# Optimization experiments

Hardware: AMD Instinct MI355X
Metric: run time of the kernel (lower is better)

Reference implementation:

```python
import jax, jax.numpy as jnp
import numpy as np

INF_MIN = -10000.0
B, S, VOCAB = 256, 1024, 126
T = VOCAB + 2           # tag_size
START, END = T - 2, T - 1


def setup_inputs() -> dict:
    key = jax.random.key(0)
    k1, k2, k3 = jax.random.split(key, 3)
    features = jax.random.normal(k1, (B, S, T), dtype=jnp.float32)
    batch_len = jax.random.randint(k2, (B,), 1, S + 1, dtype=jnp.int32)
    transitions = jax.random.normal(k3, (T, T), dtype=jnp.float32)
    # CRF structural constraints set at init: nothing transitions INTO start,
    # nothing transitions OUT of end.
    transitions = transitions.at[:, START].set(INF_MIN).at[END, :].set(INF_MIN)
    return {"features": features, "batch_len": batch_len, "transitions": transitions}


def reference(features, batch_len, transitions):
    # features: [B, S, T], batch_len: [B], transitions: [T, T]
    b, s, t = features.shape
    alpha0 = jnp.full((b, t), INF_MIN, dtype=features.dtype).at[:, START].set(0.0)
    feats_t = jnp.transpose(features, (1, 0, 2))  # [S, B, T]

    def step(carry, feats):
        alpha, rem = carry
        # score[b, i, j] = emit[b, i] + trans[i, j] + alpha[b, j]
        scores = feats[:, :, None] + transitions[None, :, :] + alpha[:, None, :]
        alpha_next = jax.nn.logsumexp(scores, axis=2)  # [B, T]
        alive = (rem > 0)[:, None]
        alpha = jnp.where(alive, alpha_next, alpha)
        return (alpha, rem - 1), None

    (alpha, _), _ = jax.lax.scan(step, (alpha0, batch_len), feats_t)
    alpha = alpha + transitions[END][None, :]
    return jax.nn.logsumexp(alpha, axis=1)  # [B]
```

## Files before the change

kernel.cpp:

```cpp
#include <hip/hip_runtime.h>

#define BB 256
#define SS 1024
#define TT 128
#define ST 126
#define EN 127
#define IMIN -10000.0f
#define L2E 1.4426950408889634f
#define LN2f 0.6931471805599453f
#define QS 40

__global__ __launch_bounds__(512, 1) void crf_fwd(const float* __restrict__ feats,
                                                  const int* __restrict__ blen,
                                                  const float* __restrict__ trans,
                                                  float* __restrict__ out)
{
    const int tid = threadIdx.x;
    const int i   = tid >> 2;
    const int q   = tid & 3;
    const int b   = blockIdx.x;

    __shared__ __align__(16) float vbuf[2][4 * QS];
    __shared__ __align__(16) float featbuf[2][8 * TT];
    __shared__ __align__(16) float wout[TT];
    __shared__ __align__(16) float red[8];

    const float* fb = feats + (size_t)b * (SS * TT);
    const int L = blen[b];

    *(float2*)(&featbuf[0][tid * 2]) = *(const float2*)(fb + tid * 2);
    float f0 = fb[i];

    float4 P[8];
    {
        const float* trow = trans + i * TT + q * 32;
        #pragma unroll
        for (int k = 0; k < 8; ++k) {
            float4 tv = *(const float4*)(trow + 4 * k);
            P[k].x = tv.x * L2E; P[k].y = tv.y * L2E;
            P[k].z = tv.z * L2E; P[k].w = tv.w * L2E;
        }
    }
    float rm = -3.4e38f;
    #pragma unroll
    for (int k = 0; k < 8; ++k)
        rm = fmaxf(rm, fmaxf(fmaxf(P[k].x, P[k].y), fmaxf(P[k].z, P[k].w)));
    rm = fmaxf(rm, __shfl_xor(rm, 1));
    rm = fmaxf(rm, __shfl_xor(rm, 2));

    float S = 0.f;
    #pragma unroll
    for (int k = 0; k < 8; ++k) {
        P[k].x = exp2f(P[k].x - rm); P[k].y = exp2f(P[k].y - rm);
        P[k].z = exp2f(P[k].z - rm); P[k].w = exp2f(P[k].w - rm);
        S += (P[k].x + P[k].y) + (P[k].z + P[k].w);
    }
    S += __shfl_xor(S, 1);
    S += __shfl_xor(S, 2);

    float rmc = fmaxf(rm, 0.f);
    float A1 = fmaf(f0, L2E, (IMIN * L2E) + rmc +
                    log2f(fmaf(S, exp2f(rm - rmc), exp2f(-rmc))));

    if (tid == 0) red[0] = A1;
    __syncthreads();
    float sh = red[0];
    if (q == 0) vbuf[0][(i >> 5) * QS + (i & 31)] = exp2f(A1 - sh);
    __syncthreads();

    int cur = 0;
    float2 fnx = *(const float2*)(fb + 8 * TT + tid * 2);

    for (int ch = 0; ; ++ch) {
        if (8 * ch + 8 < L) {
            *(float2*)(&featbuf[(ch + 1) & 1][tid * 2]) = fnx;
            int cn = min(8 * ch + 16, SS - 8);
            fnx = *(const float2*)(fb + cn * TT + tid * 2);
        }
        const int sLo = (ch == 0) ? 1 : 8 * ch;
        const int sHi = min(8 * ch + 8, L);
        for (int s = sLo; s < sHi; ++s) {
            const float* vb = &vbuf[cur][q * QS];
            float v0f = vbuf[cur][0];
            float fv  = featbuf[ch & 1][((s & 7) << 7) + i];
            float dsh = log2f(v0f);
            float cf  = exp2f(fmaf(fv, L2E, rm - dsh));

            float a0 = 0.f, a1 = 0.f, a2 = 0.f, a3 = 0.f;
            #pragma unroll
            for (int k = 0; k < 8; ++k) {
                float4 vv = *(const float4*)(vb + 4 * k);
                a0 = fmaf(P[k].x, vv.x, a0);
                a1 = fmaf(P[k].y, vv.y, a1);
                a2 = fmaf(P[k].z, vv.z, a2);
                a3 = fmaf(P[k].w, vv.w, a3);
            }
            float part = (a0 + a1) + (a2 + a3);
            part += __shfl_xor(part, 1);
            part += __shfl_xor(part, 2);

            float vn = cf * part;
            sh += dsh;
            if (q == 0) vbuf[cur ^ 1][(i >> 5) * QS + (i & 31)] = vn;
            __syncthreads();
            cur ^= 1;
        }
        if (8 * ch + 8 >= L) break;
    }

    float vL = vbuf[cur][(i >> 5) * QS + (i & 31)];
    float w  = fmaf(trans[EN * TT + i], L2E, sh + log2f(vL));
    if (q == 0) wout[i] = w;
    __syncthreads();
    if (tid < 64) {
        float w0 = wout[tid], w1 = wout[tid + 64];
        float mm = fmaxf(w0, w1);
        #pragma unroll
        for (int off = 1; off < 64; off <<= 1) mm = fmaxf(mm, __shfl_xor(mm, off));
        float ss = exp2f(w0 - mm) + exp2f(w1 - mm);
        #pragma unroll
        for (int off = 1; off < 64; off <<= 1) ss += __shfl_xor(ss, off);
        if (tid == 0) out[b] = (mm + log2f(ss)) * LN2f;
    }
}

extern "C" void kernel_launch(void* const* d_in, const int* in_sizes, int n_in,
                              void* d_out, int out_size, void* d_ws, size_t ws_size,
                              hipStream_t stream) {
    const float* feats = (const float*)d_in[0];
    const int*   blen  = (const int*)d_in[1];
    const float* trans = (const float*)d_in[2];
    float*       o     = (float*)d_out;
    crf_fwd<<<dim3(BB), dim3(512), 0, stream>>>(feats, blen, trans, o);
}
```

Measured before the change: 372.3 us.

## Rewrite CRF forward as single-wavefront kernel with fp16 dot2 and DPP reductions

Each batch item now runs on one 64-lane wavefront. Every lane owns two tag rows and keeps the exp-transition matrix packed as fp16 pairs in registers, computing the row dot products with v_dot2_f32_f16. This removes block-wide __syncthreads, shared feature staging and cross-lane partial sums from every time step. Per-step normalization uses a wave-wide max via DPP and shuffles, and the next feature is prefetched directly from global memory. The change risks fp16 precision loss in the transition and alpha values, and adds high register pressure from 128 packed registers per lane.

```diff
diff --git a/kernel.cpp b/kernel.cpp
--- a/kernel.cpp
+++ b/kernel.cpp
@@ -3,125 +3,152 @@
 #define BB 256
 #define SS 1024
 #define TT 128
-#define ST 126
 #define EN 127
 #define IMIN -10000.0f
 #define L2E 1.4426950408889634f
 #define LN2f 0.6931471805599453f
-#define QS 40
 
-__global__ __launch_bounds__(512, 1) void crf_fwd(const float* __restrict__ feats,
-                                                  const int* __restrict__ blen,
-                                                  const float* __restrict__ trans,
-                                                  float* __restrict__ out)
+typedef _Float16 half2v __attribute__((ext_vector_type(2)));
+
+__device__ __forceinline__ float fdot2(unsigned a, unsigned b, float c) {
+#if __has_builtin(__builtin_amdgcn_fdot2)
+    return __builtin_amdgcn_fdot2(__builtin_bit_cast(half2v, a),
+                                  __builtin_bit_cast(half2v, b), c, false);
+#else
+    float d;
+    asm volatile("v_dot2_f32_f16 %0, %1, %2, %3"
+                 : "=v"(d) : "v"(a), "v"(b), "v"(c));
+    return d;
+#endif
+}
+__device__ __forceinline__ unsigned pk16(float a, float b) {
+    return __builtin_bit_cast(unsigned, __builtin_amdgcn_cvt_pkrtz(a, b));
+}
+template<int CTRL>
+__device__ __forceinline__ float dpp_mov(float x) {
+    return __int_as_float(__builtin_amdgcn_update_dpp(
+        0, __float_as_int(x), CTRL, 0xF, 0xF, true));
+}
+__device__ __forceinline__ float wmax64(float x) {
+    x = fmaxf(x, dpp_mov<0xB1>(x));
+    x = fmaxf(x, dpp_mov<0x4E>(x));
+    x = fmaxf(x, dpp_mov<0x141>(x));
+    x = fmaxf(x, dpp_mov<0x140>(x));
+    x = fmaxf(x, __shfl_xor(x, 16));
+    x = fmaxf(x, __shfl_xor(x, 32));
+    return x;
+}
+__device__ __forceinline__ float wsum64(float x) {
+    x += dpp_mov<0xB1>(x);
+    x += dpp_mov<0x4E>(x);
+    x += dpp_mov<0x141>(x);
+    x += dpp_mov<0x140>(x);
+    x += __shfl_xor(x, 16);
+    x += __shfl_xor(x, 32);
+    return x;
+}
+
+__global__ __launch_bounds__(64, 1) void crf_fwd(const float* __restrict__ feats,
+                                                 const int* __restrict__ blen,
+                                                 const float* __restrict__ trans,
+                                                 float* __restrict__ out)
 {
-    const int tid = threadIdx.x;
-    const int i   = tid >> 2;
-    const int q   = tid & 3;
-    const int b   = blockIdx.x;
+    const int lane = threadIdx.x;
+    const int b    = blockIdx.x;
+    const int r0   = 2 * lane, r1 = 2 * lane + 1;
 
-    __shared__ __align__(16) float vbuf[2][4 * QS];
-    __shared__ __align__(16) float featbuf[2][8 * TT];
-    __shared__ __align__(16) float wout[TT];
-    __shared__ __align__(16) float red[8];
+    __shared__ __align__(16) unsigned vbuf[64];
 
     const float* fb = feats + (size_t)b * (SS * TT);
     const int L = blen[b];
 
-    *(float2*)(&featbuf[0][tid * 2]) = *(const float2*)(fb + tid * 2);
-    float f0 = fb[i];
+    const float* t0 = trans + (size_t)r0 * TT;
+    const float* t1 = trans + (size_t)r1 * TT;
+    float rm0 = -3.4e38f, rm1 = -3.4e38f;
+    #pragma unroll
+    for (int k = 0; k < 32; ++k) {
+        float4 a = ((const float4*)t0)[k];
+        rm0 = fmaxf(rm0, fmaxf(fmaxf(a.x, a.y), fmaxf(a.z, a.w)));
+        float4 c = ((const float4*)t1)[k];
+        rm1 = fmaxf(rm1, fmaxf(fmaxf(c.x, c.y), fmaxf(c.z, c.w)));
+    }
+    rm0 *= L2E; rm1 *= L2E;
 
-    float4 P[8];
-    {
-        const float* trow = trans + i * TT + q * 32;
-        #pragma unroll
-        for (int k = 0; k < 8; ++k) {
-            float4 tv = *(const float4*)(trow + 4 * k);
-            P[k].x = tv.x * L2E; P[k].y = tv.y * L2E;
-            P[k].z = tv.z * L2E; P[k].w = tv.w * L2E;
-        }
-    }
-    float rm = -3.4e38f;
+    unsigned P0[64], P1[64];
+    float S0 = 0.f, S1 = 0.f;
     #pragma unroll
-    for (int k = 0; k < 8; ++k)
-        rm = fmaxf(rm, fmaxf(fmaxf(P[k].x, P[k].y), fmaxf(P[k].z, P[k].w)));
-    rm = fmaxf(rm, __shfl_xor(rm, 1));
-    rm = fmaxf(rm, __shfl_xor(rm, 2));
-
-    float S = 0.f;
-    #pragma unroll
-    for (int k = 0; k < 8; ++k) {
-        P[k].x = exp2f(P[k].x - rm); P[k].y = exp2f(P[k].y - rm);
-        P[k].z = exp2f(P[k].z - rm); P[k].w = exp2f(P[k].w - rm);
-        S += (P[k].x + P[k].y) + (P[k].z + P[k].w);
-    }
-    S += __shfl_xor(S, 1);
-    S += __shfl_xor(S, 2);
-
-    float rmc = fmaxf(rm, 0.f);
-    float A1 = fmaf(f0, L2E, (IMIN * L2E) + rmc +
-                    log2f(fmaf(S, exp2f(rm - rmc), exp2f(-rmc))));
-
-    if (tid == 0) red[0] = A1;
-    __syncthreads();
-    float sh = red[0];
-    if (q == 0) vbuf[0][(i >> 5) * QS + (i & 31)] = exp2f(A1 - sh);
-    __syncthreads();
-
-    int cur = 0;
-    float2 fnx = *(const float2*)(fb + 8 * TT + tid * 2);
-
-    for (int ch = 0; ; ++ch) {
-        if (8 * ch + 8 < L) {
-            *(float2*)(&featbuf[(ch + 1) & 1][tid * 2]) = fnx;
-            int cn = min(8 * ch + 16, SS - 8);
-            fnx = *(const float2*)(fb + cn * TT + tid * 2);
-        }
-        const int sLo = (ch == 0) ? 1 : 8 * ch;
-        const int sHi = min(8 * ch + 8, L);
-        for (int s = sLo; s < sHi; ++s) {
-            const float* vb = &vbuf[cur][q * QS];
-            float v0f = vbuf[cur][0];
-            float fv  = featbuf[ch & 1][((s & 7) << 7) + i];
-            float dsh = log2f(v0f);
-            float cf  = exp2f(fmaf(fv, L2E, rm - dsh));
-
-            float a0 = 0.f, a1 = 0.f, a2 = 0.f, a3 = 0.f;
-            #pragma unroll
-            for (int k = 0; k < 8; ++k) {
-                float4 vv = *(const float4*)(vb + 4 * k);
-                a0 = fmaf(P[k].x, vv.x, a0);
-                a1 = fmaf(P[k].y, vv.y, a1);
-                a2 = fmaf(P[k].z, vv.z, a2);
-                a3 = fmaf(P[k].w, vv.w, a3);
-            }
-            float part = (a0 + a1) + (a2 + a3);
-            part += __shfl_xor(part, 1);
-            part += __shfl_xor(part, 2);
-
-            float vn = cf * part;
-            sh += dsh;
-            if (q == 0) vbuf[cur ^ 1][(i >> 5) * QS + (i & 31)] = vn;
-            __syncthreads();
-            cur ^= 1;
-        }
-        if (8 * ch + 8 >= L) break;
+    for (int k = 0; k < 32; ++k) {
+        float4 a = ((const float4*)t0)[k];
+        float e0 = exp2f(fmaf(a.x, L2E, -rm0)), e1 = exp2f(fmaf(a.y, L2E, -rm0));
+        float e2 = exp2f(fmaf(a.z, L2E, -rm0)), e3 = exp2f(fmaf(a.w, L2E, -rm0));
+        S0 += (e0 + e1) + (e2 + e3);
+        P0[2 * k] = pk16(e0, e1); P0[2 * k + 1] = pk16(e2, e3);
+        float4 c = ((const float4*)t1)[k];
+        float g0 = exp2f(fmaf(c.x, L2E, -rm1)), g1 = exp2f(fmaf(c.y, L2E, -rm1));
+        float g2 = exp2f(fmaf(c.z, L2E, -rm1)), g3 = exp2f(fmaf(c.w, L2E, -rm1));
+        S1 += (g0 + g1) + (g2 + g3);
+        P1[2 * k] = pk16(g0, g1); P1[2 * k + 1] = pk16(g2, g3);
     }
 
-    float vL = vbuf[cur][(i >> 5) * QS + (i & 31)];
-    float w  = fmaf(trans[EN * TT + i], L2E, sh + log2f(vL));
-    if (q == 0) wout[i] = w;
-    __syncthreads();
-    if (tid < 64) {
-        float w0 = wout[tid], w1 = wout[tid + 64];
-        float mm = fmaxf(w0, w1);
+    float2 f0 = *(const float2*)(fb + r0);
+    float rmc0 = fmaxf(rm0, 0.f), rmc1 = fmaxf(rm1, 0.f);
+    float A10 = fmaf(f0.x, L2E, (IMIN * L2E) + rmc0 +
+                     log2f(fmaf(S0, exp2f(rm0 - rmc0), exp2f(-rmc0))));
+    float A11 = fmaf(f0.y, L2E, (IMIN * L2E) + rmc1 +
+                     log2f(fmaf(S1, exp2f(rm1 - rmc1), exp2f(-rmc1))));
+
+    float m0 = wmax64(fmaxf(A10, A11));
+    float sh = m0;
+    float vf0 = exp2f(A10 - m0), vf1 = exp2f(A11 - m0);
+    vbuf[lane] = pk16(vf0, vf1);
+
+    float2 fcur = *(const float2*)(fb + TT + r0);
+    for (int s = 1; s < L; ++s) {
+        int sn = (s + 1 < SS) ? s + 1 : SS - 1;
+        float2 fnx = *(const float2*)(fb + (size_t)sn * TT + r0);
+        asm volatile("" :: "v"(fnx.x), "v"(fnx.y));
+
+        uint4 VA[16];
+        const uint4* vv = (const uint4*)vbuf;
         #pragma unroll
-        for (int off = 1; off < 64; off <<= 1) mm = fmaxf(mm, __shfl_xor(mm, off));
-        float ss = exp2f(w0 - mm) + exp2f(w1 - mm);
+        for (int p = 0; p < 16; ++p) VA[p] = vv[p];
+
+        float ef0 = exp2f(fmaf(fcur.x, L2E, rm0));
+        float ef1 = exp2f(fmaf(fcur.y, L2E, rm1));
+
+        float a0 = 0.f, a1 = 0.f, a2 = 0.f, a3 = 0.f;
+        float b0 = 0.f, b1 = 0.f, b2 = 0.f, b3 = 0.f;
         #pragma unroll
-        for (int off = 1; off < 64; off <<= 1) ss += __shfl_xor(ss, off);
-        if (tid == 0) out[b] = (mm + log2f(ss)) * LN2f;
+        for (int p = 0; p < 16; ++p) {
+            a0 = fdot2(P0[4 * p + 0], VA[p].x, a0);
+            a1 = fdot2(P0[4 * p + 1], VA[p].y, a1);
+            a2 = fdot2(P0[4 * p + 2], VA[p].z, a2);
+            a3 = fdot2(P0[4 * p + 3], VA[p].w, a3);
+            b0 = fdot2(P1[4 * p + 0], VA[p].x, b0);
+            b1 = fdot2(P1[4 * p + 1], VA[p].y, b1);
+            b2 = fdot2(P1[4 * p + 2], VA[p].z, b2);
+            b3 = fdot2(P1[4 * p + 3], VA[p].w, b3);
+        }
+        float u0 = (a0 + a1) + (a2 + a3);
+        float u1 = (b0 + b1) + (b2 + b3);
+        float y0 = ef0 * u0, y1 = ef1 * u1;
+
+        float m = wmax64(fmaxf(y0, y1));
+        float rinv = __builtin_amdgcn_rcpf(m);
+        vf0 = y0 * rinv; vf1 = y1 * rinv;
+        sh += log2f(m);
+        vbuf[lane] = pk16(vf0, vf1);
+        fcur = fnx;
     }
+
+    float A0 = sh + log2f(vf0);
+    float A1e = sh + log2f(vf1);
+    float w0 = fmaf(trans[(size_t)EN * TT + r0], L2E, A0);
+    float w1 = fmaf(trans[(size_t)EN * TT + r1], L2E, A1e);
+    float mm = wmax64(fmaxf(w0, w1));
+    float e  = exp2f(w0 - mm) + exp2f(w1 - mm);
+    float ss = wsum64(e);
+    if (lane == 0) out[b] = (mm + log2f(ss)) * LN2f;
 }
 
 extern "C" void kernel_launch(void* const* d_in, const int* in_sizes, int n_in,
@@ -131,5 +158,5 @@
     const int*   blen  = (const int*)d_in[1];
     const float* trans = (const float*)d_in[2];
     float*       o     = (float*)d_out;
-    crf_fwd<<<dim3(BB), dim3(512), 0, stream>>>(feats, blen, trans, o);
+    crf_fwd<<<dim3(BB), dim3(64), 0, stream>>>(feats, blen, trans, o);
 }
```

Measured after the change: 717.5 us. +92.7%, slower.
